# Kernel tuning notes

Hardware: AMD Instinct MI355X
Metric: run time of the kernel (lower is better)

The kernel has to match this reference:

```python
import jax, jax.numpy as jnp
import numpy as np

TOPK = 10  # keep N // TOPK largest scores per query row
EPS = 1e-10


def setup_inputs() -> dict:
    key = jax.random.key(0)
    ks = jax.random.split(key, 8)
    B, C, H, W = 4, 64, 64, 64
    KD, OD = 32, 64  # key_dim, out_dim (out_dim must equal C for residual/view)
    x = jax.random.normal(ks[0], (B, C, H, W), jnp.float32)
    s = 0.05
    Wq = jax.random.normal(ks[1], (KD, C), jnp.float32) * s
    bq = jax.random.normal(ks[2], (KD,), jnp.float32) * s
    Wk = jax.random.normal(ks[3], (KD, C), jnp.float32) * s
    bk = jax.random.normal(ks[4], (KD,), jnp.float32) * s
    Wv = jax.random.normal(ks[5], (OD, C), jnp.float32) * s
    bv = jax.random.normal(ks[6], (OD,), jnp.float32) * s
    gamma = jnp.full((1,), 0.5, jnp.float32)  # torch init is 0; nonzero so output != x
    return {"x": x, "Wq": Wq, "bq": bq, "Wk": Wk, "bk": bk, "Wv": Wv, "bv": bv, "gamma": gamma}


def reference(x, Wq, bq, Wk, bk, Wv, bv, gamma):
    B, C, H, W = x.shape
    N = H * W
    xf = x.reshape(B, C, N)
    # 1x1 convs == per-pixel linear projections
    q = jnp.einsum('kc,bcn->bnk', Wq, xf) + bq                 # [B, N, KD]
    k = jnp.einsum('kc,bcn->bkn', Wk, xf) + bk[:, None]        # [B, KD, N]
    v = jnp.einsum('vc,bcn->bvn', Wv, xf) + bv[:, None]        # [B, OD, N]
    energy = jnp.einsum('bnk,bkm->bnm', q, k)                  # [B, N, N]
    kk = N // TOPK
    _, idx = jax.lax.top_k(energy, kk)                         # [B, N, kk]
    # scatter 1.0 at top-k positions along last dim
    bi = jnp.arange(B)[:, None, None]
    ri = jnp.arange(N)[None, :, None]
    mask = jnp.zeros_like(energy).at[bi, ri, idx].set(1.0)
    # mask_softmax: max over FULL row (matches torch code), exp, mask, renormalize
    m = jnp.max(energy, axis=-1, keepdims=True)
    e = jnp.exp(energy - m) * mask
    attn = e / (jnp.sum(e, axis=-1, keepdims=True) + EPS)      # [B, N, N]
    # bmm(value, attention^T): out[b,v,i] = sum_j v[b,v,j] * attn[b,i,j]
    out = jnp.einsum('bvj,bij->bvi', v, attn)                  # [B, OD, N]
    return (gamma[0] * out + xf).reshape(B, C, H, W)
```

## Files before the change

### kernel.cpp

```cpp
#include <hip/hip_runtime.h>

#define BATCH 4
#define CCH   64
#define NPIX  4096
#define KD    32
#define OD    64
#define KK    409
#define EPSF  1e-10f

__global__ __launch_bounds__(256) void qkv_kernel(
    const float* __restrict__ x,
    const float* __restrict__ Wq, const float* __restrict__ bq,
    const float* __restrict__ Wk, const float* __restrict__ bk,
    const float* __restrict__ Wv, const float* __restrict__ bv,
    float* __restrict__ Q, float* __restrict__ Km, float* __restrict__ Vm)
{
    __shared__ float xt[64][65];
    __shared__ float wq_s[KD * 64];
    __shared__ float wk_s[KD * 64];
    __shared__ float wv_s[OD * 64];
    __shared__ float bq_s[KD], bk_s[KD], bv_s[OD];

    int tid = threadIdx.x;
    int bx  = blockIdx.x;
    int b   = bx >> 6;
    int n0  = (bx & 63) << 6;

    for (int i = tid; i < KD * 64; i += 256) { wq_s[i] = Wq[i]; wk_s[i] = Wk[i]; }
    for (int i = tid; i < OD * 64; i += 256) wv_s[i] = Wv[i];
    if (tid < KD) { bq_s[tid] = bq[tid]; bk_s[tid] = bk[tid]; }
    if (tid < OD) bv_s[tid] = bv[tid];
    for (int i = tid; i < 64 * 64; i += 256) {
        int c = i >> 6, p = i & 63;
        xt[c][p] = x[((size_t)b * CCH + c) * NPIX + n0 + p];
    }
    __syncthreads();

    int px  = tid & 63;
    int grp = tid >> 6;
    int n   = n0 + px;

    if (grp == 0) {
        for (int o = 0; o < KD; ++o) {
            float acc = bq_s[o];
            #pragma unroll
            for (int c = 0; c < 64; ++c) acc += wq_s[o * 64 + c] * xt[c][px];
            Q[((size_t)b * NPIX + n) * KD + o] = acc;
        }
    } else if (grp == 1) {
        for (int o = 0; o < KD; ++o) {
            float acc = bk_s[o];
            #pragma unroll
            for (int c = 0; c < 64; ++c) acc += wk_s[o * 64 + c] * xt[c][px];
            Km[((size_t)b * KD + o) * NPIX + n] = acc;
        }
    } else {
        int obase = (grp - 2) * 32;
        for (int oo = 0; oo < 32; ++oo) {
            int o = obase + oo;
            float acc = bv_s[o];
            #pragma unroll
            for (int c = 0; c < 64; ++c) acc += wv_s[o * 64 + c] * xt[c][px];
            Vm[((size_t)b * NPIX + n) * OD + o] = acc;
        }
    }
}

__global__ __launch_bounds__(256, 2) void attn_kernel(
    const float* __restrict__ x,  const float* __restrict__ Q,
    const float* __restrict__ Km, const float* __restrict__ Vm,
    const float* __restrict__ gamma, float* __restrict__ out)
{
    __shared__ __align__(16) unsigned short ek[4][NPIX];
    __shared__ __align__(16) float qld[KD][4];
    __shared__ __align__(16) unsigned h4[4][256];
    __shared__ unsigned redk0[4][4];
    volatile __shared__ unsigned sh_b4[4], sh_r4[4];

    int tid  = threadIdx.x;
    int lane = tid & 63, wv = tid >> 6;
    int bx   = blockIdx.x;
    int b    = bx >> 10;
    int i0   = (bx & 1023) << 2;

    float gscale = gamma[0];

    if (tid < 128) {
        int kd = tid & 31, rr = tid >> 5;
        qld[kd][rr] = Q[((size_t)b * NPIX + i0 + rr) * KD + kd];
    }
    __syncthreads();

    #define EKEY(EV, KV) { KV = (int)fmaf((EV), 4096.0f, 32768.0f); \
                           KV = KV < 0 ? 0 : (KV > 65535 ? 65535 : KV); }

    const float4* Kb4 = (const float4*)(Km + (size_t)b * KD * NPIX);
    unsigned lmax0 = 0u, lmax1 = 0u, lmax2 = 0u, lmax3 = 0u;
    #pragma unroll 1
    for (int g = 0; g < 4; ++g) {
        int c4 = tid + (g << 8);
        float4 a0 = {0,0,0,0}, a1 = {0,0,0,0}, a2 = {0,0,0,0}, a3 = {0,0,0,0};
        #pragma unroll 4
        for (int kd = 0; kd < KD; ++kd) {
            float4 kv = Kb4[(kd << 10) + c4];
            float4 qv = *(const float4*)qld[kd];
            a0.x = fmaf(qv.x, kv.x, a0.x); a0.y = fmaf(qv.x, kv.y, a0.y);
            a0.z = fmaf(qv.x, kv.z, a0.z); a0.w = fmaf(qv.x, kv.w, a0.w);
            a1.x = fmaf(qv.y, kv.x, a1.x); a1.y = fmaf(qv.y, kv.y, a1.y);
            a1.z = fmaf(qv.y, kv.z, a1.z); a1.w = fmaf(qv.y, kv.w, a1.w);
            a2.x = fmaf(qv.z, kv.x, a2.x); a2.y = fmaf(qv.z, kv.y, a2.y);
            a2.z = fmaf(qv.z, kv.z, a2.z); a2.w = fmaf(qv.z, kv.w, a2.w);
            a3.x = fmaf(qv.w, kv.x, a3.x); a3.y = fmaf(qv.w, kv.y, a3.y);
            a3.z = fmaf(qv.w, kv.z, a3.z); a3.w = fmaf(qv.w, kv.w, a3.w);
        }
        #define DOROW(A, R, LM) { int k0,k1,k2,k3; \
            EKEY(A.x,k0); EKEY(A.y,k1); EKEY(A.z,k2); EKEY(A.w,k3); \
            LM = max(LM, (unsigned)max(max(k0,k1),max(k2,k3))); \
            ((ushort4*)ek[R])[c4] = make_ushort4((unsigned short)k0,(unsigned short)k1, \
                                                 (unsigned short)k2,(unsigned short)k3); }
        DOROW(a0, 0, lmax0) DOROW(a1, 1, lmax1) DOROW(a2, 2, lmax2) DOROW(a3, 3, lmax3)
        #undef DOROW
    }
    #define RMAX(V, R) { unsigned v_ = (V); \
        _Pragma("unroll") \
        for (int off = 32; off; off >>= 1) \
            v_ = max(v_, (unsigned)__shfl_down((int)v_, off, 64)); \
        if (lane == 0) redk0[wv][R] = v_; }
    RMAX(lmax0, 0) RMAX(lmax1, 1) RMAX(lmax2, 2) RMAX(lmax3, 3)
    #undef RMAX
    __syncthreads();

    const int r = wv;
    const int i = i0 + r;
    unsigned mk = max(max(redk0[0][r], redk0[1][r]), max(redk0[2][r], redk0[3][r]));
    const ushort4* ek4 = (const ushort4*)ek[r];
    unsigned* hw = h4[r];

    #define WSCAN(RNEED, OUTB, OUTR) { \
        uint4 hh = *((const uint4*)&hw[lane << 2]); \
        unsigned s3 = hh.w, s2 = hh.w + hh.z, s1 = s2 + hh.y, s0 = s1 + hh.x; \
        unsigned X = s0; \
        _Pragma("unroll") \
        for (int off = 1; off < 64; off <<= 1) { \
            unsigned v = (unsigned)__shfl_down((int)X, off, 64); \
            if (lane + off < 64) X += v; } \
        unsigned Xn = (unsigned)__shfl_down((int)X, 1, 64); \
        if (lane == 63) Xn = 0u; \
        unsigned S0 = X, S1 = Xn + s1, S2 = Xn + s2, S3 = Xn + s3, S4 = Xn; \
        if (S0 >= (RNEED) && S1 < (RNEED)) { sh_b4[r] = (lane << 2) | 0; sh_r4[r] = (RNEED) - S1; } \
        if (S1 >= (RNEED) && S2 < (RNEED)) { sh_b4[r] = (lane << 2) | 1; sh_r4[r] = (RNEED) - S2; } \
        if (S2 >= (RNEED) && S3 < (RNEED)) { sh_b4[r] = (lane << 2) | 2; sh_r4[r] = (RNEED) - S3; } \
        if (S3 >= (RNEED) && S4 < (RNEED)) { sh_b4[r] = (lane << 2) | 3; sh_r4[r] = (RNEED) - S4; } \
        OUTB = sh_b4[r]; OUTR = sh_r4[r]; }

    #pragma unroll
    for (int z = 0; z < 4; ++z) hw[(z << 6) + lane] = 0u;
    #pragma unroll 4
    for (int g = 0; g < 16; ++g) {
        ushort4 kv = ek4[lane + (g << 6)];
        atomicAdd(&hw[kv.x >> 8], 1u);
        atomicAdd(&hw[kv.y >> 8], 1u);
        atomicAdd(&hw[kv.z >> 8], 1u);
        atomicAdd(&hw[kv.w >> 8], 1u);
    }
    unsigned bh, rn;
    WSCAN(KK, bh, rn)

    #pragma unroll
    for (int z = 0; z < 4; ++z) hw[(z << 6) + lane] = 0u;
    #pragma unroll 4
    for (int g = 0; g < 16; ++g) {
        ushort4 kv = ek4[lane + (g << 6)];
        if ((unsigned)(kv.x >> 8) == bh) atomicAdd(&hw[kv.x & 255u], 1u);
        if ((unsigned)(kv.y >> 8) == bh) atomicAdd(&hw[kv.y & 255u], 1u);
        if ((unsigned)(kv.z >> 8) == bh) atomicAdd(&hw[kv.z & 255u], 1u);
        if ((unsigned)(kv.w >> 8) == bh) atomicAdd(&hw[kv.w & 255u], 1u);
    }
    unsigned bl, rt;
    WSCAN(rn, bl, rt)
    #undef WSCAN
    int tu = (int)((bh << 8) | bl);

    unsigned short* selr = (unsigned short*)hw;
    unsigned base = 0u, tbase = 0u;
    float lsum = 0.f;
    #pragma unroll 4
    for (int g = 0; g < 16; ++g) {
        ushort4 kv = ek4[lane + (g << 6)];
        #pragma unroll
        for (int c = 0; c < 4; ++c) {
            int k = (c == 0) ? kv.x : (c == 1) ? kv.y : (c == 2) ? kv.z : kv.w;
            bool tie = (k == tu);
            unsigned long long tmask = __ballot(tie);
            bool sel = (k > tu);
            if (tie) {
                unsigned tix = tbase + (unsigned)__popcll(tmask & ((1ull << lane) - 1ull));
                sel = (tix < rt);
            }
            tbase += (unsigned)__popcll(tmask);
            unsigned long long smask = __ballot(sel);
            if (sel) {
                unsigned pos = base + (unsigned)__popcll(smask & ((1ull << lane) - 1ull));
                int j = ((lane + (g << 6)) << 2) | c;
                selr[pos] = (unsigned short)j;
                lsum += __expf((float)(k - (int)mk) * 0.000244140625f);
            }
            base += (unsigned)__popcll(smask);
        }
    }
    #pragma unroll
    for (int off = 32; off; off >>= 1) lsum += __shfl_xor(lsum, off, 64);
    float denom = lsum + EPSF;

    int eslot = lane >> 4, vq = lane & 15;
    const float4* Vb4 = (const float4*)(Vm + (size_t)b * NPIX * OD);
    const unsigned short* ekr = ek[r];
    float4 acc = make_float4(0.f, 0.f, 0.f, 0.f);
    #pragma unroll 1
    for (int s0 = 0; s0 < KK; s0 += 4) {
        int s = s0 + eslot;
        if (s < KK) {
            int j = selr[s];
            int k = ekr[j];
            float w = __expf((float)(k - (int)mk) * 0.000244140625f);
            float4 v4 = Vb4[(j << 4) + vq];
            acc.x = fmaf(w, v4.x, acc.x);
            acc.y = fmaf(w, v4.y, acc.y);
            acc.z = fmaf(w, v4.z, acc.z);
            acc.w = fmaf(w, v4.w, acc.w);
        }
    }
    #pragma unroll
    for (int off = 16; off <= 32; off <<= 1) {
        acc.x += __shfl_xor(acc.x, off, 64);
        acc.y += __shfl_xor(acc.y, off, 64);
        acc.z += __shfl_xor(acc.z, off, 64);
        acc.w += __shfl_xor(acc.w, off, 64);
    }
    if (lane < 16) {
        float sc = gscale / denom;
        size_t basei = ((size_t)b * CCH + (vq << 2)) * NPIX + i;
        out[basei]            = fmaf(sc, acc.x, x[basei]);
        out[basei +   NPIX]   = fmaf(sc, acc.y, x[basei +   NPIX]);
        out[basei + 2*NPIX]   = fmaf(sc, acc.z, x[basei + 2*NPIX]);
        out[basei + 3*NPIX]   = fmaf(sc, acc.w, x[basei + 3*NPIX]);
    }
}

extern "C" void kernel_launch(void* const* d_in, const int* in_sizes, int n_in,
                              void* d_out, int out_size, void* d_ws, size_t ws_size,
                              hipStream_t stream) {
    const float* x     = (const float*)d_in[0];
    const float* Wq    = (const float*)d_in[1];
    const float* bq    = (const float*)d_in[2];
    const float* Wk    = (const float*)d_in[3];
    const float* bk    = (const float*)d_in[4];
    const float* Wv    = (const float*)d_in[5];
    const float* bv    = (const float*)d_in[6];
    const float* gamma = (const float*)d_in[7];
    float* out = (float*)d_out;

    float* Q  = (float*)d_ws;
    float* Km = Q  + (size_t)BATCH * NPIX * KD;
    float* Vm = Km + (size_t)BATCH * KD * NPIX;

    qkv_kernel<<<BATCH * (NPIX / 64), 256, 0, stream>>>(x, Wq, bq, Wk, bk, Wv, bv, Q, Km, Vm);
    attn_kernel<<<BATCH * (NPIX / 4), 256, 0, stream>>>(x, Q, Km, Vm, gamma, out);
}
```

Before: 323.6 us.

## Process eight query rows per attention block and restructure QKV projection into register tiles

The attention kernel now handles 8 query rows per 512-thread block instead of 4, so each K tile loaded from global memory feeds twice as many rows. The energy-key buffer grows to 64KB of LDS per block. The QKV kernel is split into separate Q/K blocks and V blocks, with transposed weights in LDS and 16 outputs accumulated in registers per thread, which reduces LDS weight reads. The V-gather loop is also unrolled by 2. Larger blocks and the extra accumulators raise register and LDS pressure, which may lower occupancy.

```diff
diff --git a/kernel.cpp b/kernel.cpp
--- a/kernel.cpp
+++ b/kernel.cpp
@@ -8,7 +8,7 @@
 #define KK    409
 #define EPSF  1e-10f
 
-__global__ __launch_bounds__(256) void qkv_kernel(
+__global__ __launch_bounds__(256, 4) void qkv_kernel(
     const float* __restrict__ x,
     const float* __restrict__ Wq, const float* __restrict__ bq,
     const float* __restrict__ Wk, const float* __restrict__ bk,
@@ -16,76 +16,101 @@
     float* __restrict__ Q, float* __restrict__ Km, float* __restrict__ Vm)
 {
     __shared__ float xt[64][65];
-    __shared__ float wq_s[KD * 64];
-    __shared__ float wk_s[KD * 64];
-    __shared__ float wv_s[OD * 64];
-    __shared__ float bq_s[KD], bk_s[KD], bv_s[OD];
+    __shared__ float wat[64][36];
+    __shared__ float wbt[64][36];
+    __shared__ float ba_s[32], bb_s[32];
 
     int tid = threadIdx.x;
     int bx  = blockIdx.x;
-    int b   = bx >> 6;
-    int n0  = (bx & 63) << 6;
-
-    for (int i = tid; i < KD * 64; i += 256) { wq_s[i] = Wq[i]; wk_s[i] = Wk[i]; }
-    for (int i = tid; i < OD * 64; i += 256) wv_s[i] = Wv[i];
-    if (tid < KD) { bq_s[tid] = bq[tid]; bk_s[tid] = bk[tid]; }
-    if (tid < OD) bv_s[tid] = bv[tid];
+    bool vmode = bx >= 256;
+    int tile = vmode ? bx - 256 : bx;
+    int b    = tile >> 6;
+    int n0   = (tile & 63) << 6;
+
     for (int i = tid; i < 64 * 64; i += 256) {
         int c = i >> 6, p = i & 63;
         xt[c][p] = x[((size_t)b * CCH + c) * NPIX + n0 + p];
     }
+    if (!vmode) {
+        for (int i = tid; i < 2048; i += 256) {
+            int o = i >> 6, c = i & 63;
+            wat[c][o] = Wq[i];
+            wbt[c][o] = Wk[i];
+        }
+        if (tid < 32) { ba_s[tid] = bq[tid]; bb_s[tid] = bk[tid]; }
+    } else {
+        for (int i = tid; i < 4096; i += 256) {
+            int o = i >> 6, c = i & 63;
+            if (o < 32) wat[c][o] = Wv[i]; else wbt[c][o - 32] = Wv[i];
+        }
+        if (tid < 32) { ba_s[tid] = bv[tid]; bb_s[tid] = bv[tid + 32]; }
+    }
     __syncthreads();
 
     int px  = tid & 63;
     int grp = tid >> 6;
     int n   = n0 + px;
-
-    if (grp == 0) {
-        for (int o = 0; o < KD; ++o) {
-            float acc = bq_s[o];
+    const float (*wt)[36] = (grp < 2) ? wat : wbt;
+    const float* bs = (grp < 2) ? ba_s : bb_s;
+    int o0 = (grp & 1) << 4;
+
+    float a[16];
+    #pragma unroll
+    for (int t = 0; t < 16; ++t) a[t] = bs[o0 + t];
+
+    #pragma unroll 2
+    for (int c = 0; c < 64; ++c) {
+        float xv = xt[c][px];
+        const float4* wr = (const float4*)&wt[c][o0];
+        float4 w0 = wr[0], w1 = wr[1], w2 = wr[2], w3 = wr[3];
+        a[0]  = fmaf(w0.x, xv, a[0]);  a[1]  = fmaf(w0.y, xv, a[1]);
+        a[2]  = fmaf(w0.z, xv, a[2]);  a[3]  = fmaf(w0.w, xv, a[3]);
+        a[4]  = fmaf(w1.x, xv, a[4]);  a[5]  = fmaf(w1.y, xv, a[5]);
+        a[6]  = fmaf(w1.z, xv, a[6]);  a[7]  = fmaf(w1.w, xv, a[7]);
+        a[8]  = fmaf(w2.x, xv, a[8]);  a[9]  = fmaf(w2.y, xv, a[9]);
+        a[10] = fmaf(w2.z, xv, a[10]); a[11] = fmaf(w2.w, xv, a[11]);
+        a[12] = fmaf(w3.x, xv, a[12]); a[13] = fmaf(w3.y, xv, a[13]);
+        a[14] = fmaf(w3.z, xv, a[14]); a[15] = fmaf(w3.w, xv, a[15]);
+    }
+
+    if (!vmode) {
+        if (grp < 2) {
             #pragma unroll
-            for (int c = 0; c < 64; ++c) acc += wq_s[o * 64 + c] * xt[c][px];
-            Q[((size_t)b * NPIX + n) * KD + o] = acc;
-        }
-    } else if (grp == 1) {
-        for (int o = 0; o < KD; ++o) {
-            float acc = bk_s[o];
+            for (int t = 0; t < 16; ++t)
+                Q[((size_t)b * NPIX + n) * KD + o0 + t] = a[t];
+        } else {
             #pragma unroll
-            for (int c = 0; c < 64; ++c) acc += wk_s[o * 64 + c] * xt[c][px];
-            Km[((size_t)b * KD + o) * NPIX + n] = acc;
+            for (int t = 0; t < 16; ++t)
+                Km[((size_t)b * KD + o0 + t) * NPIX + n] = a[t];
         }
     } else {
-        int obase = (grp - 2) * 32;
-        for (int oo = 0; oo < 32; ++oo) {
-            int o = obase + oo;
-            float acc = bv_s[o];
-            #pragma unroll
-            for (int c = 0; c < 64; ++c) acc += wv_s[o * 64 + c] * xt[c][px];
-            Vm[((size_t)b * NPIX + n) * OD + o] = acc;
-        }
+        int ob = ((grp < 2) ? 0 : 32) + o0;
+        #pragma unroll
+        for (int t = 0; t < 16; ++t)
+            Vm[((size_t)b * NPIX + n) * OD + ob + t] = a[t];
     }
 }
 
-__global__ __launch_bounds__(256, 2) void attn_kernel(
+__global__ __launch_bounds__(512, 4) void attn_kernel(
     const float* __restrict__ x,  const float* __restrict__ Q,
     const float* __restrict__ Km, const float* __restrict__ Vm,
     const float* __restrict__ gamma, float* __restrict__ out)
 {
-    __shared__ __align__(16) unsigned short ek[4][NPIX];
-    __shared__ __align__(16) float qld[KD][4];
-    __shared__ __align__(16) unsigned h4[4][256];
-    __shared__ unsigned redk0[4][4];
-    volatile __shared__ unsigned sh_b4[4], sh_r4[4];
+    __shared__ __align__(16) unsigned short ek[8][NPIX];
+    __shared__ __align__(16) float qld[KD][8];
+    __shared__ __align__(16) unsigned h8[8][256];
+    __shared__ unsigned redk0[8][8];
+    volatile __shared__ unsigned sh_b8[8], sh_r8[8];
 
     int tid  = threadIdx.x;
     int lane = tid & 63, wv = tid >> 6;
     int bx   = blockIdx.x;
-    int b    = bx >> 10;
-    int i0   = (bx & 1023) << 2;
+    int b    = bx >> 9;
+    int i0   = (bx & 511) << 3;
 
     float gscale = gamma[0];
 
-    if (tid < 128) {
+    if (tid < 256) {
         int kd = tid & 31, rr = tid >> 5;
         qld[kd][rr] = Q[((size_t)b * NPIX + i0 + rr) * KD + kd];
     }
@@ -95,30 +120,31 @@
                            KV = KV < 0 ? 0 : (KV > 65535 ? 65535 : KV); }
 
     const float4* Kb4 = (const float4*)(Km + (size_t)b * KD * NPIX);
-    unsigned lmax0 = 0u, lmax1 = 0u, lmax2 = 0u, lmax3 = 0u;
+    unsigned lm0 = 0u, lm1 = 0u, lm2 = 0u, lm3 = 0u,
+             lm4 = 0u, lm5 = 0u, lm6 = 0u, lm7 = 0u;
     #pragma unroll 1
-    for (int g = 0; g < 4; ++g) {
-        int c4 = tid + (g << 8);
+    for (int g = 0; g < 2; ++g) {
+        int c4 = tid + (g << 9);
         float4 a0 = {0,0,0,0}, a1 = {0,0,0,0}, a2 = {0,0,0,0}, a3 = {0,0,0,0};
+        float4 a4 = {0,0,0,0}, a5 = {0,0,0,0}, a6 = {0,0,0,0}, a7 = {0,0,0,0};
         #pragma unroll 4
         for (int kd = 0; kd < KD; ++kd) {
             float4 kv = Kb4[(kd << 10) + c4];
-            float4 qv = *(const float4*)qld[kd];
-            a0.x = fmaf(qv.x, kv.x, a0.x); a0.y = fmaf(qv.x, kv.y, a0.y);
-            a0.z = fmaf(qv.x, kv.z, a0.z); a0.w = fmaf(qv.x, kv.w, a0.w);
-            a1.x = fmaf(qv.y, kv.x, a1.x); a1.y = fmaf(qv.y, kv.y, a1.y);
-            a1.z = fmaf(qv.y, kv.z, a1.z); a1.w = fmaf(qv.y, kv.w, a1.w);
-            a2.x = fmaf(qv.z, kv.x, a2.x); a2.y = fmaf(qv.z, kv.y, a2.y);
-            a2.z = fmaf(qv.z, kv.z, a2.z); a2.w = fmaf(qv.z, kv.w, a2.w);
-            a3.x = fmaf(qv.w, kv.x, a3.x); a3.y = fmaf(qv.w, kv.y, a3.y);
-            a3.z = fmaf(qv.w, kv.z, a3.z); a3.w = fmaf(qv.w, kv.w, a3.w);
+            float4 qA = *(const float4*)&qld[kd][0];
+            float4 qB = *(const float4*)&qld[kd][4];
+            #define FMA4(A, S) { A.x = fmaf((S), kv.x, A.x); A.y = fmaf((S), kv.y, A.y); \
+                                 A.z = fmaf((S), kv.z, A.z); A.w = fmaf((S), kv.w, A.w); }
+            FMA4(a0, qA.x) FMA4(a1, qA.y) FMA4(a2, qA.z) FMA4(a3, qA.w)
+            FMA4(a4, qB.x) FMA4(a5, qB.y) FMA4(a6, qB.z) FMA4(a7, qB.w)
+            #undef FMA4
         }
         #define DOROW(A, R, LM) { int k0,k1,k2,k3; \
             EKEY(A.x,k0); EKEY(A.y,k1); EKEY(A.z,k2); EKEY(A.w,k3); \
             LM = max(LM, (unsigned)max(max(k0,k1),max(k2,k3))); \
             ((ushort4*)ek[R])[c4] = make_ushort4((unsigned short)k0,(unsigned short)k1, \
                                                  (unsigned short)k2,(unsigned short)k3); }
-        DOROW(a0, 0, lmax0) DOROW(a1, 1, lmax1) DOROW(a2, 2, lmax2) DOROW(a3, 3, lmax3)
+        DOROW(a0,0,lm0) DOROW(a1,1,lm1) DOROW(a2,2,lm2) DOROW(a3,3,lm3)
+        DOROW(a4,4,lm4) DOROW(a5,5,lm5) DOROW(a6,6,lm6) DOROW(a7,7,lm7)
         #undef DOROW
     }
     #define RMAX(V, R) { unsigned v_ = (V); \
@@ -126,15 +152,18 @@
         for (int off = 32; off; off >>= 1) \
             v_ = max(v_, (unsigned)__shfl_down((int)v_, off, 64)); \
         if (lane == 0) redk0[wv][R] = v_; }
-    RMAX(lmax0, 0) RMAX(lmax1, 1) RMAX(lmax2, 2) RMAX(lmax3, 3)
+    RMAX(lm0,0) RMAX(lm1,1) RMAX(lm2,2) RMAX(lm3,3)
+    RMAX(lm4,4) RMAX(lm5,5) RMAX(lm6,6) RMAX(lm7,7)
     #undef RMAX
     __syncthreads();
 
     const int r = wv;
     const int i = i0 + r;
-    unsigned mk = max(max(redk0[0][r], redk0[1][r]), max(redk0[2][r], redk0[3][r]));
+    unsigned mk = 0u;
+    #pragma unroll
+    for (int w = 0; w < 8; ++w) mk = max(mk, redk0[w][r]);
     const ushort4* ek4 = (const ushort4*)ek[r];
-    unsigned* hw = h4[r];
+    unsigned* hw = h8[r];
 
     #define WSCAN(RNEED, OUTB, OUTR) { \
         uint4 hh = *((const uint4*)&hw[lane << 2]); \
@@ -147,11 +176,11 @@
         unsigned Xn = (unsigned)__shfl_down((int)X, 1, 64); \
         if (lane == 63) Xn = 0u; \
         unsigned S0 = X, S1 = Xn + s1, S2 = Xn + s2, S3 = Xn + s3, S4 = Xn; \
-        if (S0 >= (RNEED) && S1 < (RNEED)) { sh_b4[r] = (lane << 2) | 0; sh_r4[r] = (RNEED) - S1; } \
-        if (S1 >= (RNEED) && S2 < (RNEED)) { sh_b4[r] = (lane << 2) | 1; sh_r4[r] = (RNEED) - S2; } \
-        if (S2 >= (RNEED) && S3 < (RNEED)) { sh_b4[r] = (lane << 2) | 2; sh_r4[r] = (RNEED) - S3; } \
-        if (S3 >= (RNEED) && S4 < (RNEED)) { sh_b4[r] = (lane << 2) | 3; sh_r4[r] = (RNEED) - S4; } \
-        OUTB = sh_b4[r]; OUTR = sh_r4[r]; }
+        if (S0 >= (RNEED) && S1 < (RNEED)) { sh_b8[r] = (lane << 2) | 0; sh_r8[r] = (RNEED) - S1; } \
+        if (S1 >= (RNEED) && S2 < (RNEED)) { sh_b8[r] = (lane << 2) | 1; sh_r8[r] = (RNEED) - S2; } \
+        if (S2 >= (RNEED) && S3 < (RNEED)) { sh_b8[r] = (lane << 2) | 2; sh_r8[r] = (RNEED) - S3; } \
+        if (S3 >= (RNEED) && S4 < (RNEED)) { sh_b8[r] = (lane << 2) | 3; sh_r8[r] = (RNEED) - S4; } \
+        OUTB = sh_b8[r]; OUTR = sh_r8[r]; }
 
     #pragma unroll
     for (int z = 0; z < 4; ++z) hw[(z << 6) + lane] = 0u;
@@ -216,7 +245,7 @@
     const float4* Vb4 = (const float4*)(Vm + (size_t)b * NPIX * OD);
     const unsigned short* ekr = ek[r];
     float4 acc = make_float4(0.f, 0.f, 0.f, 0.f);
-    #pragma unroll 1
+    #pragma unroll 2
     for (int s0 = 0; s0 < KK; s0 += 4) {
         int s = s0 + eslot;
         if (s < KK) {
@@ -264,6 +293,6 @@
     float* Km = Q  + (size_t)BATCH * NPIX * KD;
     float* Vm = Km + (size_t)BATCH * KD * NPIX;
 
-    qkv_kernel<<<BATCH * (NPIX / 64), 256, 0, stream>>>(x, Wq, bq, Wk, bk, Wv, bv, Q, Km, Vm);
-    attn_kernel<<<BATCH * (NPIX / 4), 256, 0, stream>>>(x, Q, Km, Vm, gamma, out);
+    qkv_kernel<<<512, 256, 0, stream>>>(x, Wq, bq, Wk, bk, Wv, bv, Q, Km, Vm);
+    attn_kernel<<<BATCH * (NPIX / 8), 512, 0, stream>>>(x, Q, Km, Vm, gamma, out);
 }
```

After: 317.5 us. Within noise of the previous version (-1.9%).
